# Kernel optimization log

Measured on AMD Instinct MI355X. Metric: run time of the kernel, lower is better.

The kernel has to match this reference:

```python
import jax, jax.numpy as jnp
import numpy as np

HIDDEN = 5120
N_HEADS = 16           # 128 total heads / DEVICE_NUM=8
Q_LORA = 1536
KV_LORA = 512
NOPE = 128
ROPE = 64
QK_DIM = NOPE + ROPE   # 192
V_DIM = 128
EPS = 1e-6
ROPE_BASE = 10000.0
SCALE_BY_DEVICE = 1.0 / 8.0
SOFTMAX_SCALE = QK_DIM ** -0.5
B, S = 1, 2048


def rms_norm(x, w, eps=EPS):
    v = jnp.mean(jnp.square(x), axis=-1, keepdims=True)
    return x * jax.lax.rsqrt(v + eps) * w


def rotate_half(x):
    h = x.shape[-1] // 2
    return jnp.concatenate([-x[..., h:], x[..., :h]], axis=-1)


def interleave(x):
    # DeepSeek rope layout: view(b,h,s,d//2,2).transpose(-1,-2).reshape(b,h,s,d)
    b, h, s, d = x.shape
    return jnp.swapaxes(x.reshape(b, h, s, d // 2, 2), -1, -2).reshape(b, h, s, d)


def setup_inputs() -> dict:
    key = jax.random.key(0)
    ks = jax.random.split(key, 8)
    w = 0.02
    hidden_states = jax.random.normal(ks[0], (B, S, HIDDEN), dtype=jnp.float32)
    position_ids = jnp.arange(S, dtype=jnp.int64 if jax.config.jax_enable_x64 else jnp.int32)[None, :]
    causal = jnp.tril(jnp.ones((S, S), dtype=bool))
    attention_mask = jnp.where(causal, 0.0, -1e9).astype(jnp.float32)[None, None]
    return {
        'hidden_states': hidden_states,
        'position_ids': position_ids,
        'attention_mask': attention_mask,
        'ln_w': jnp.ones((HIDDEN,), jnp.float32),
        'wq_a': jax.random.normal(ks[1], (Q_LORA, HIDDEN), jnp.float32) * w,
        'q_a_ln_w': jnp.ones((Q_LORA,), jnp.float32),
        'wq_b': jax.random.normal(ks[2], (N_HEADS * QK_DIM, Q_LORA), jnp.float32) * w,
        'wkv_a': jax.random.normal(ks[3], (KV_LORA + ROPE, HIDDEN), jnp.float32) * w,
        'kv_a_ln_w': jnp.ones((KV_LORA,), jnp.float32),
        'wkv_b': jax.random.normal(ks[4], (N_HEADS * (NOPE + V_DIM), KV_LORA), jnp.float32) * w,
        'wo': jax.random.normal(ks[5], (HIDDEN, N_HEADS * V_DIM), jnp.float32) * w,
    }


def reference(hidden_states, position_ids, attention_mask, ln_w, wq_a, q_a_ln_w,
              wq_b, wkv_a, kv_a_ln_w, wkv_b, wo):
    b, s, _ = hidden_states.shape
    residual = hidden_states * SCALE_BY_DEVICE
    h = rms_norm(hidden_states, ln_w)

    # Q low-rank decompression: q_a_proj -> RMSNorm -> q_b_proj
    q = rms_norm(h @ wq_a.T, q_a_ln_w) @ wq_b.T
    q = q.reshape(b, s, N_HEADS, QK_DIM).transpose(0, 2, 1, 3)  # b,h,s,192
    q_nope, q_pe = q[..., :NOPE], q[..., NOPE:]

    # KV low-rank: kv_a_proj_with_mqa -> split -> RMSNorm -> kv_b_proj
    ckv = h @ wkv_a.T                                           # b,s,512+64
    c_kv, k_pe = ckv[..., :KV_LORA], ckv[..., KV_LORA:]
    k_pe = k_pe[:, None, :, :]                                  # b,1,s,64
    kv = rms_norm(c_kv, kv_a_ln_w) @ wkv_b.T
    kv = kv.reshape(b, s, N_HEADS, NOPE + V_DIM).transpose(0, 2, 1, 3)
    k_nope, v = kv[..., :NOPE], kv[..., NOPE:]

    # RoPE (DeepSeek interleaved layout)
    inv_freq = 1.0 / (ROPE_BASE ** (jnp.arange(0, ROPE, 2, dtype=jnp.float32) / ROPE))
    freqs = position_ids.astype(jnp.float32)[..., None] * inv_freq  # b,s,32
    emb = jnp.concatenate([freqs, freqs], axis=-1)                  # b,s,64
    cos = jnp.cos(emb)[:, None]                                     # b,1,s,64
    sin = jnp.sin(emb)[:, None]
    q_pe = interleave(q_pe)
    k_pe = interleave(k_pe)
    q_pe = q_pe * cos + rotate_half(q_pe) * sin
    k_pe = k_pe * cos + rotate_half(k_pe) * sin

    k = jnp.concatenate([k_nope, jnp.broadcast_to(k_pe, (b, N_HEADS, s, ROPE))], axis=-1)
    qf = jnp.concatenate([q_nope, q_pe], axis=-1)

    scores = jnp.einsum('bhqd,bhkd->bhqk', qf, k) * SOFTMAX_SCALE + attention_mask
    attn = jax.nn.softmax(scores.astype(jnp.float32), axis=-1).astype(qf.dtype)
    out = jnp.einsum('bhqk,bhkd->bhqd', attn, v)                    # b,h,s,128
    out = out.transpose(0, 2, 1, 3).reshape(b, s, N_HEADS * V_DIM) @ wo.T

    hidden_states = residual + out
    return (hidden_states.astype(jnp.float32), k.astype(jnp.float32), v.astype(jnp.float32))
```

## Files before the change

kernel.cpp:

```cpp
#include <hip/hip_runtime.h>
#include <hip/hip_bf16.h>

typedef __hip_bfloat16 bf16;
typedef __attribute__((ext_vector_type(8))) short bf16x8;
typedef __attribute__((ext_vector_type(4))) float f32x4;

#define S_LEN   2048
#define HIDDEN  5120
#define NHEADS  16
#define QLORA   1536
#define KVLORA  512
#define QKD     192
#define VD      128
#define QN      (NHEADS*QKD)
#define KVN     (NHEADS*(128+VD))
#define QCKN    2112
#define SM_SCALE 0.07216878364870322f

__device__ __forceinline__ f32x4 mfma16(bf16x8 a, bf16x8 b, f32x4 c) {
  return __builtin_amdgcn_mfma_f32_16x16x32_bf16(a, b, c, 0, 0, 0);
}
__device__ __forceinline__ void g2l16(const void* g, void* l) {
  __builtin_amdgcn_global_load_lds((const __attribute__((address_space(1))) void*)g,
                                   (__attribute__((address_space(3))) void*)l, 16, 0, 0);
}
__device__ __forceinline__ bf16x8 ld8(const bf16* p) { return *(const bf16x8*)p; }

__global__ void cvt_multi(const float* s0, bf16* d0, int n0,
                          const float* s1, bf16* d1, int n1,
                          const float* s2, bf16* d2, int n2,
                          const float* s3, bf16* d3, int n3,
                          const float* s4, bf16* d4, int n4s)
{
  int i = blockIdx.x * 256 + threadIdx.x;
  const float* s; bf16* d;
  if (i < n0) { s = s0; d = d0; }
  else if ((i -= n0) < n1) { s = s1; d = d1; }
  else if ((i -= n1) < n2) { s = s2; d = d2; }
  else if ((i -= n2) < n3) { s = s3; d = d3; }
  else if ((i -= n3) < n4s) { s = s4; d = d4; }
  else return;
  const float4 v = ((const float4*)s)[i];
  union { bf16 b[4]; unsigned long long u; } pk;
  pk.b[0] = __float2bfloat16(v.x);
  pk.b[1] = __float2bfloat16(v.y);
  pk.b[2] = __float2bfloat16(v.z);
  pk.b[3] = __float2bfloat16(v.w);
  *(unsigned long long*)(d + (size_t)i * 4) = pk.u;
}

__global__ void rmsnorm_k(const float* __restrict__ in, int istride, int C,
                          const float* __restrict__ w,
                          bf16* __restrict__ out, int ostride)
{
  const int row = blockIdx.x;
  const float* x = in + (size_t)row * istride;
  float ss = 0.f;
  for (int c = threadIdx.x; c < C; c += 256) { float v = x[c]; ss += v * v; }
  #pragma unroll
  for (int m = 32; m >= 1; m >>= 1) ss += __shfl_xor(ss, m, 64);
  __shared__ float red[4];
  if ((threadIdx.x & 63) == 0) red[threadIdx.x >> 6] = ss;
  __syncthreads();
  ss = red[0] + red[1] + red[2] + red[3];
  const float sc = rsqrtf(ss / (float)C + 1e-6f);
  bf16* o = out + (size_t)row * ostride;
  for (int c = threadIdx.x; c < C; c += 256)
    o[c] = __float2bfloat16(x[c] * sc * w[c]);
}

__global__ void rmsnorm2_k(const float* __restrict__ parts,
                           const float* __restrict__ wq, const float* __restrict__ wk,
                           bf16* __restrict__ qa_n, bf16* __restrict__ ckv_n,
                           float* __restrict__ kpe_sum)
{
  const int r = blockIdx.x;
  const bool is_q = r < S_LEN;
  const int row = is_q ? r : r - S_LEN;
  const int C = is_q ? QLORA : KVLORA;
  const size_t PS = (size_t)S_LEN * QCKN;
  const float* x0 = parts + (size_t)row * QCKN + (is_q ? 0 : QLORA);
  const float* w = is_q ? wq : wk;
  bf16* o = (is_q ? qa_n + (size_t)row * QLORA : ckv_n + (size_t)row * KVLORA);
  __shared__ float xs[QLORA];
  float ss = 0.f;
  for (int c = threadIdx.x; c < C; c += 256) {
    const float v = x0[c] + x0[PS + c] + x0[2 * PS + c] + x0[3 * PS + c];
    xs[c] = v;
    ss += v * v;
  }
  #pragma unroll
  for (int m = 32; m >= 1; m >>= 1) ss += __shfl_xor(ss, m, 64);
  __shared__ float red[4];
  if ((threadIdx.x & 63) == 0) red[threadIdx.x >> 6] = ss;
  __syncthreads();
  ss = red[0] + red[1] + red[2] + red[3];
  const float sc = rsqrtf(ss / (float)C + 1e-6f);
  for (int c = threadIdx.x; c < C; c += 256)
    o[c] = __float2bfloat16(xs[c] * sc * w[c]);
  if (!is_q) {
    const float* kp = parts + (size_t)row * QCKN + 2048;
    for (int c = threadIdx.x; c < 64; c += 256)
      kpe_sum[row * 64 + c] = kp[c] + kp[PS + c] + kp[2 * PS + c] + kp[3 * PS + c];
  }
}

template<bool RESID, bool CLAMPN, bool SPLIT>
__global__ __launch_bounds__(256, 4)
void gemm_nt(const bf16* __restrict__ A, const bf16* __restrict__ Bt,
             float* __restrict__ C, int M, int N, int lda, int klen,
             const float* __restrict__ resid, float rscale)
{
  __shared__ bf16 As[2 * 128 * 32];
  __shared__ bf16 Bs[2 * 128 * 32];
  const int tid = threadIdx.x;
  const int wave = tid >> 6;
  const int lane = tid & 63;
  const int l15 = lane & 15, quad = lane >> 4;
  const int bm = blockIdx.x * 128, bn = blockIdx.y * 128;
  const int kbase = blockIdx.z * klen;
  const int wm = (wave >> 1) * 64, wn = (wave & 1) * 64;

  const int srow = tid >> 2;
  const int scol = (((tid & 3) ^ ((tid >> 3) & 3)) << 3);
  const bf16* Ag0 = A + (size_t)(bm + srow) * lda + kbase + scol;
  const bf16* Ag1 = A + (size_t)(bm + 64 + srow) * lda + kbase + scol;
  int bn0 = bn + srow, bn1 = bn + 64 + srow;
  if (CLAMPN) { bn0 = min(bn0, N - 1); bn1 = min(bn1, N - 1); }
  const bf16* Bg0 = Bt + (size_t)bn0 * lda + kbase + scol;
  const bf16* Bg1 = Bt + (size_t)bn1 * lda + kbase + scol;

  char* AsW = (char*)As + wave * 1024;
  char* BsW = (char*)Bs + wave * 1024;

  const int qs = ((quad ^ ((l15 >> 1) & 3)) << 3);

  f32x4 acc[4][4];
  #pragma unroll
  for (int i = 0; i < 4; i++)
    #pragma unroll
    for (int j = 0; j < 4; j++) acc[i][j] = (f32x4){0.f, 0.f, 0.f, 0.f};

  const int nk = klen >> 6;
  for (int kt = 0; kt < nk; ++kt) {
    const int k0 = kt << 6;
    #pragma unroll
    for (int c = 0; c < 2; ++c) {
      g2l16(Ag0 + k0 + c * 32, AsW + c * 8192);
      g2l16(Ag1 + k0 + c * 32, AsW + c * 8192 + 4096);
      g2l16(Bg0 + k0 + c * 32, BsW + c * 8192);
      g2l16(Bg1 + k0 + c * 32, BsW + c * 8192 + 4096);
    }
    __syncthreads();
    #pragma unroll
    for (int c = 0; c < 2; ++c) {
      bf16x8 af[4], bfr[4];
      #pragma unroll
      for (int i = 0; i < 4; i++)
        af[i] = ld8(As + c * 4096 + (wm + i * 16 + l15) * 32 + qs);
      #pragma unroll
      for (int j = 0; j < 4; j++)
        bfr[j] = ld8(Bs + c * 4096 + (wn + j * 16 + l15) * 32 + qs);
      #pragma unroll
      for (int i = 0; i < 4; i++)
        #pragma unroll
        for (int j = 0; j < 4; j++)
          acc[i][j] = mfma16(af[i], bfr[j], acc[i][j]);
    }
    __syncthreads();
  }

  float* Cb = C;
  if (SPLIT) Cb += (size_t)blockIdx.z * ((size_t)S_LEN * (size_t)N);
  #pragma unroll
  for (int i = 0; i < 4; i++)
    #pragma unroll
    for (int j = 0; j < 4; j++) {
      const int row = bm + wm + i * 16 + quad * 4;
      const int col = bn + wn + j * 16 + l15;
      if (!CLAMPN || col < N) {
        #pragma unroll
        for (int r = 0; r < 4; r++) {
          float v = acc[i][j][r];
          const size_t idx = (size_t)(row + r) * N + col;
          if (RESID) v += resid[idx] * rscale;
          Cb[idx] = v;
        }
      }
    }
}

__global__ void rope_assemble_k(
    const float* __restrict__ qp,
    const float* __restrict__ kpe_sum,
    const float* __restrict__ kv,
    const int*   __restrict__ pos,
    float* __restrict__ k_out,
    bf16*  __restrict__ q_bf,
    bf16*  __restrict__ k_bf)
{
  const int s = blockIdx.x;
  const int t = threadIdx.x;
  const size_t QPS = (size_t)S_LEN * QN;
  __shared__ float cs[32], sn[32], kpe[64];
  const float p = (float)pos[s];
  if (t < 32) {
    const float inv = powf(10000.0f, -((float)(2 * t)) / 64.0f);
    const float f = p * inv;
    float si, c;
    sincosf(f, &si, &c);
    cs[t] = c; sn[t] = si;
    const float r0v = kpe_sum[(size_t)s * 64 + 2 * t];
    const float r1v = kpe_sum[(size_t)s * 64 + 2 * t + 1];
    kpe[t]      = r0v * c - r1v * si;
    kpe[32 + t] = r1v * c + r0v * si;
  }
  __syncthreads();
  for (int i = t; i < NHEADS * 128; i += 256) {
    const int h = i >> 7, d = i & 127;
    const size_t o = ((size_t)h * S_LEN + s) * QKD + d;
    const float kn = kv[(size_t)s * KVN + h * 256 + d];
    k_out[o] = kn;
    k_bf[o] = __float2bfloat16(kn);
    const size_t qi = (size_t)s * QN + h * QKD + d;
    q_bf[o] = __float2bfloat16(qp[qi] + qp[QPS + qi]);
  }
  for (int i = t; i < NHEADS * 32; i += 256) {
    const int h = i >> 5, jj = i & 31;
    const size_t qi = (size_t)s * QN + h * QKD + 128 + 2 * jj;
    const float r0v = qp[qi] + qp[QPS + qi];
    const float r1v = qp[qi + 1] + qp[QPS + qi + 1];
    const float c = cs[jj], si = sn[jj];
    const size_t o = ((size_t)h * S_LEN + s) * QKD + 128;
    q_bf[o + jj]      = __float2bfloat16(r0v * c - r1v * si);
    q_bf[o + 32 + jj] = __float2bfloat16(r1v * c + r0v * si);
  }
  for (int i = t; i < NHEADS * 64; i += 256) {
    const int h = i >> 6, jj = i & 63;
    const float v = kpe[jj];
    const size_t o = ((size_t)h * S_LEN + s) * QKD + 128 + jj;
    k_out[o] = v;
    k_bf[o] = __float2bfloat16(v);
  }
}

__global__ void v_transpose_k(const float* __restrict__ kv,
                              float* __restrict__ v_out,
                              bf16* __restrict__ vt_bf)
{
  const int h = blockIdx.x, st = blockIdx.y, dt = blockIdx.z;
  __shared__ float tile[32][33];
  const int tx = threadIdx.x & 31;
  const int ty = (threadIdx.x >> 5) * 4;
  const int s0 = st * 32, d0 = dt * 32;
  #pragma unroll
  for (int r = 0; r < 4; r++) {
    const int sl = ty + r;
    const float v = kv[(size_t)(s0 + sl) * KVN + h * 256 + 128 + d0 + tx];
    v_out[((size_t)h * S_LEN + s0 + sl) * VD + d0 + tx] = v;
    tile[sl][tx] = v;
  }
  __syncthreads();
  #pragma unroll
  for (int r = 0; r < 4; r++) {
    const int dl = ty + r;
    vt_bf[((size_t)h * VD + d0 + dl) * S_LEN + s0 + tx] = __float2bfloat16(tile[tx][dl]);
  }
}

template<bool PARTIAL>
__device__ __forceinline__ void attn_tile(
    const bf16* __restrict__ qh, const bf16* __restrict__ kh,
    const bf16* __restrict__ vh,
    bf16* Ks, bf16* Vs, bf16* Plds,
    int qt, int j0, int j1, int head,
    bf16* __restrict__ aout, float* __restrict__ Op, float* __restrict__ Ml)
{
  const int tid = threadIdx.x;
  const int wave = tid >> 6, lane = tid & 63;
  const int l15 = lane & 15, quad = lane >> 4;
  const int r0 = qt * 64 + wave * 16;

  const int srow = wave * 16 + (lane >> 2);
  const int scol = (lane & 3) * 8;
  const bf16* ksrc = kh + (size_t)srow * QKD + scol;
  bf16* kdst = Ks + srow * 32 + (((lane & 3) ^ ((lane >> 3) & 3)) << 3);
  const int vrow = tid >> 1;
  const int vcol = (tid & 1) * 32;
  const bf16* vsrc = vh + (size_t)vrow * S_LEN + vcol;
  bf16* vdst = Vs + vrow * 72 + vcol;
  const int qs = ((quad ^ ((l15 >> 1) & 3)) << 3);

  bf16x8 qf[6];
  #pragma unroll
  for (int c = 0; c < 6; ++c)
    qf[c] = ld8(qh + (size_t)(r0 + l15) * QKD + c * 32 + quad * 8);

  f32x4 O[8];
  #pragma unroll
  for (int d = 0; d < 8; ++d) O[d] = (f32x4){0.f, 0.f, 0.f, 0.f};
  float mrow[4] = {-1e30f, -1e30f, -1e30f, -1e30f};
  float lrow[4] = {0.f, 0.f, 0.f, 0.f};

  bf16x8 kreg[6], vreg[4];
  #pragma unroll
  for (int c = 0; c < 6; ++c) kreg[c] = ld8(ksrc + (size_t)j0 * 64 * QKD + c * 32);
  #pragma unroll
  for (int c = 0; c < 4; ++c) vreg[c] = ld8(vsrc + (size_t)j0 * 64 + c * 8);

  for (int j = j0; j < j1; ++j) {
    __syncthreads();
    #pragma unroll
    for (int c = 0; c < 6; ++c) *(bf16x8*)(kdst + c * 2048) = kreg[c];
    #pragma unroll
    for (int c = 0; c < 4; ++c) *(bf16x8*)(vdst + c * 8) = vreg[c];
    __syncthreads();
    if (j + 1 < j1) {
      const bf16* src = ksrc + (size_t)(j + 1) * 64 * QKD;
      #pragma unroll
      for (int c = 0; c < 6; ++c) kreg[c] = ld8(src + c * 32);
      const bf16* vs2 = vsrc + (size_t)(j + 1) * 64;
      #pragma unroll
      for (int c = 0; c < 4; ++c) vreg[c] = ld8(vs2 + c * 8);
    }
    const int kc = j * 64;

    f32x4 S[4];
    #pragma unroll
    for (int nt = 0; nt < 4; ++nt) S[nt] = (f32x4){0.f, 0.f, 0.f, 0.f};
    #pragma unroll
    for (int c = 0; c < 6; ++c)
      #pragma unroll
      for (int nt = 0; nt < 4; ++nt) {
        const bf16x8 kf = ld8(Ks + c * 2048 + (nt * 16 + l15) * 32 + qs);
        S[nt] = mfma16(qf[c], kf, S[nt]);
      }

    float mnew[4] = {-1e30f, -1e30f, -1e30f, -1e30f};
    if (j == qt) {
      #pragma unroll
      for (int nt = 0; nt < 4; ++nt) {
        const int col = kc + nt * 16 + l15;
        #pragma unroll
        for (int r = 0; r < 4; r++) {
          const int row = r0 + quad * 4 + r;
          const float v = (col <= row) ? S[nt][r] * SM_SCALE : -1e30f;
          S[nt][r] = v;
          mnew[r] = fmaxf(mnew[r], v);
        }
      }
    } else {
      #pragma unroll
      for (int nt = 0; nt < 4; ++nt)
        #pragma unroll
        for (int r = 0; r < 4; r++) {
          const float v = S[nt][r] * SM_SCALE;
          S[nt][r] = v;
          mnew[r] = fmaxf(mnew[r], v);
        }
    }
    #pragma unroll
    for (int m = 8; m >= 1; m >>= 1)
      #pragma unroll
      for (int r = 0; r < 4; r++)
        mnew[r] = fmaxf(mnew[r], __shfl_xor(mnew[r], m, 64));
    float alpha[4], ladd[4] = {0.f, 0.f, 0.f, 0.f};
    #pragma unroll
    for (int r = 0; r < 4; r++) {
      const float mi = fmaxf(mrow[r], mnew[r]);
      alpha[r] = __expf(mrow[r] - mi);
      mrow[r] = mi;
    }
    #pragma unroll
    for (int nt = 0; nt < 4; ++nt)
      #pragma unroll
      for (int r = 0; r < 4; r++) {
        const float pv = __expf(S[nt][r] - mrow[r]);
        S[nt][r] = pv;
        ladd[r] += pv;
      }
    #pragma unroll
    for (int m = 8; m >= 1; m >>= 1)
      #pragma unroll
      for (int r = 0; r < 4; r++) ladd[r] += __shfl_xor(ladd[r], m, 64);
    #pragma unroll
    for (int r = 0; r < 4; r++) lrow[r] = lrow[r] * alpha[r] + ladd[r];
    #pragma unroll
    for (int d = 0; d < 8; ++d)
      #pragma unroll
      for (int r = 0; r < 4; r++) O[d][r] *= alpha[r];

    #pragma unroll
    for (int nt = 0; nt < 4; ++nt)
      #pragma unroll
      for (int r = 0; r < 4; r++)
        Plds[(wave * 16 + quad * 4 + r) * 72 + nt * 16 + l15] =
            __float2bfloat16(S[nt][r]);

    #pragma unroll
    for (int kt = 0; kt < 2; ++kt) {
      const bf16x8 pf = ld8(Plds + (wave * 16 + l15) * 72 + kt * 32 + quad * 8);
      #pragma unroll
      for (int dt = 0; dt < 8; ++dt) {
        const bf16x8 vf = ld8(Vs + (dt * 16 + l15) * 72 + kt * 32 + quad * 8);
        O[dt] = mfma16(pf, vf, O[dt]);
      }
    }
  }

  if (PARTIAL) {
    #pragma unroll
    for (int dt = 0; dt < 8; ++dt)
      #pragma unroll
      for (int r = 0; r < 4; r++)
        Op[(wave * 16 + quad * 4 + r) * 128 + dt * 16 + l15] = O[dt][r];
    if (l15 == 0) {
      #pragma unroll
      for (int r = 0; r < 4; r++) {
        Ml[wave * 16 + quad * 4 + r] = mrow[r];
        Ml[64 + wave * 16 + quad * 4 + r] = lrow[r];
      }
    }
  } else {
    #pragma unroll
    for (int dt = 0; dt < 8; ++dt) {
      const int col = head * VD + dt * 16 + l15;
      #pragma unroll
      for (int r = 0; r < 4; r++) {
        const int row = r0 + quad * 4 + r;
        aout[(size_t)row * (NHEADS * VD) + col] = __float2bfloat16(O[dt][r] / lrow[r]);
      }
    }
  }
}

__global__ __launch_bounds__(256, 2)
void attn_k(const bf16* __restrict__ qb, const bf16* __restrict__ kb,
            const bf16* __restrict__ vt, bf16* __restrict__ aout,
            float* __restrict__ Opart, float* __restrict__ Mlpart)
{
  __shared__ bf16 Ks[6 * 64 * 32];
  __shared__ bf16 Vs[128 * 72];
  __shared__ bf16 Plds[4 * 16 * 72];

  const int lin = blockIdx.x;
  const int xcd = lin & 7;
  const int t = lin >> 3;
  const int head = xcd * 2 + (t >> 5);
  const int rem = t & 31;
  const int b = rem >> 1;
  const int role = rem & 1;
  const int qtl = b, qth = 31 - b;
  const int pi = head * 16 + (15 - b);

  const bf16* qh = qb + (size_t)head * S_LEN * QKD;
  const bf16* kh = kb + (size_t)head * S_LEN * QKD;
  const bf16* vh = vt + (size_t)head * VD * S_LEN;

  if (role == 0) {
    attn_tile<true>(qh, kh, vh, Ks, Vs, Plds, qth, 0, 16, head, aout,
                    Opart + (size_t)pi * 8192, Mlpart + (size_t)pi * 128);
  } else {
    attn_tile<false>(qh, kh, vh, Ks, Vs, Plds, qtl, 0, qtl + 1, head, aout,
                     nullptr, nullptr);
    attn_tile<true>(qh, kh, vh, Ks, Vs, Plds, qth, 16, qth + 1, head, aout,
                    Opart + (size_t)(256 + pi) * 8192,
                    Mlpart + (size_t)(256 + pi) * 128);
  }
}

__global__ void merge_k(const float* __restrict__ Opart,
                        const float* __restrict__ Mlpart,
                        bf16* __restrict__ aout)
{
  const int pi = blockIdx.x;
  const int head = pi >> 4;
  const int qth = (pi & 15) + 16;
  const int tid = threadIdx.x;
  const int r = tid >> 2;
  const int d0 = (tid & 3) * 32;
  const float mA = Mlpart[(size_t)pi * 128 + r];
  const float lA = Mlpart[(size_t)pi * 128 + 64 + r];
  const float mB = Mlpart[(size_t)(256 + pi) * 128 + r];
  const float lB = Mlpart[(size_t)(256 + pi) * 128 + 64 + r];
  const float m = fmaxf(mA, mB);
  const float fa = __expf(mA - m), fb = __expf(mB - m);
  const float inv = 1.f / (lA * fa + lB * fb);
  const float4* OA = (const float4*)(Opart + (size_t)pi * 8192 + r * 128 + d0);
  const float4* OB = (const float4*)(Opart + (size_t)(256 + pi) * 8192 + r * 128 + d0);
  bf16* out = aout + (size_t)(qth * 64 + r) * (NHEADS * VD) + head * VD + d0;
  #pragma unroll
  for (int i = 0; i < 8; ++i) {
    const float4 va = OA[i], vb = OB[i];
    union { bf16 h[4]; unsigned long long u; } pk;
    pk.h[0] = __float2bfloat16((va.x * fa + vb.x * fb) * inv);
    pk.h[1] = __float2bfloat16((va.y * fa + vb.y * fb) * inv);
    pk.h[2] = __float2bfloat16((va.z * fa + vb.z * fb) * inv);
    pk.h[3] = __float2bfloat16((va.w * fa + vb.w * fb) * inv);
    *(unsigned long long*)(out + i * 4) = pk.u;
  }
}

extern "C" void kernel_launch(void* const* d_in, const int* in_sizes, int n_in,
                              void* d_out, int out_size, void* d_ws, size_t ws_size,
                              hipStream_t stream)
{
  const float* hs      = (const float*)d_in[0];
  const int*   pos     = (const int*)  d_in[1];
  const float* ln_w    = (const float*)d_in[3];
  const float* wq_a    = (const float*)d_in[4];
  const float* q_a_ln  = (const float*)d_in[5];
  const float* wq_b    = (const float*)d_in[6];
  const float* wkv_a   = (const float*)d_in[7];
  const float* kv_a_ln = (const float*)d_in[8];
  const float* wkv_b   = (const float*)d_in[9];
  const float* wo      = (const float*)d_in[10];

  float* out_hidden = (float*)d_out;
  float* out_k = out_hidden + (size_t)S_LEN * HIDDEN;
  float* out_v = out_k + (size_t)NHEADS * S_LEN * QKD;

  char* ws = (char*)d_ws;
  size_t off = 0;
  auto alloc = [&](size_t bytes) { char* p = ws + off; off += (bytes + 255) & ~255ULL; return p; };

  bf16* h_b     = (bf16*)alloc((size_t)S_LEN * HIDDEN * 2);
  bf16* w1_b    = (bf16*)alloc((size_t)QCKN * HIDDEN * 2);
  bf16* wqb_b   = (bf16*)alloc((size_t)QN * QLORA * 2);
  bf16* wkvb_b  = (bf16*)alloc((size_t)KVN * KVLORA * 2);
  bf16* wo_b    = (bf16*)alloc((size_t)HIDDEN * (NHEADS * VD) * 2);
  char* region  = alloc((size_t)2 * S_LEN * QN * 4 + (size_t)S_LEN * KVN * 4);
  float* qa_parts = (float*)region;
  float* q_f      = (float*)region;
  float* kv_f     = (float*)(region + (size_t)2 * S_LEN * QN * 4);
  float* Opart    = (float*)region;
  float* Mlpart   = (float*)(region + (size_t)512 * 8192 * 4);
  float* kpe_sum = (float*)alloc((size_t)S_LEN * 64 * 4);
  bf16* qa_n    = (bf16*)alloc((size_t)S_LEN * QLORA * 2);
  bf16* ckv_n   = (bf16*)alloc((size_t)S_LEN * KVLORA * 2);
  bf16* q_bf    = (bf16*)alloc((size_t)NHEADS * S_LEN * QKD * 2);
  bf16* k_bf    = (bf16*)alloc((size_t)NHEADS * S_LEN * QKD * 2);
  bf16* vt_bf   = (bf16*)alloc((size_t)NHEADS * VD * S_LEN * 2);
  bf16* attn_b  = (bf16*)alloc((size_t)S_LEN * (NHEADS * VD) * 2);

  {
    const int n0 = (QLORA * HIDDEN) / 4;
    const int n1 = ((QCKN - QLORA) * HIDDEN) / 4;
    const int n2 = (QN * QLORA) / 4;
    const int n3 = (KVN * KVLORA) / 4;
    const int n4s = (HIDDEN * NHEADS * VD) / 4;
    const int tot = n0 + n1 + n2 + n3 + n4s;
    cvt_multi<<<(tot + 255) / 256, 256, 0, stream>>>(
        wq_a, w1_b, n0,
        wkv_a, w1_b + (size_t)QLORA * HIDDEN, n1,
        wq_b, wqb_b, n2,
        wkv_b, wkvb_b, n3,
        wo, wo_b, n4s);
  }

  rmsnorm_k<<<S_LEN, 256, 0, stream>>>(hs, HIDDEN, HIDDEN, ln_w, h_b, HIDDEN);

  gemm_nt<false, true, true><<<dim3(16, 17, 4), 256, 0, stream>>>(
      h_b, w1_b, qa_parts, S_LEN, QCKN, HIDDEN, HIDDEN / 4, nullptr, 0.f);

  rmsnorm2_k<<<2 * S_LEN, 256, 0, stream>>>(qa_parts, q_a_ln, kv_a_ln,
                                            qa_n, ckv_n, kpe_sum);

  gemm_nt<false, false, true><<<dim3(16, QN / 128, 2), 256, 0, stream>>>(
      qa_n, wqb_b, q_f, S_LEN, QN, QLORA, QLORA / 2, nullptr, 0.f);
  gemm_nt<false, false, false><<<dim3(16, KVN / 128, 1), 256, 0, stream>>>(
      ckv_n, wkvb_b, kv_f, S_LEN, KVN, KVLORA, KVLORA, nullptr, 0.f);

  rope_assemble_k<<<S_LEN, 256, 0, stream>>>(q_f, kpe_sum, kv_f, pos,
                                             out_k, q_bf, k_bf);
  v_transpose_k<<<dim3(NHEADS, S_LEN / 32, VD / 32), 256, 0, stream>>>(kv_f, out_v, vt_bf);

  attn_k<<<dim3(512), 256, 0, stream>>>(q_bf, k_bf, vt_bf, attn_b, Opart, Mlpart);
  merge_k<<<dim3(256), 256, 0, stream>>>(Opart, Mlpart, attn_b);

  gemm_nt<true, false, false><<<dim3(16, HIDDEN / 128, 1), 256, 0, stream>>>(
      attn_b, wo_b, out_hidden, S_LEN, HIDDEN, NHEADS * VD, NHEADS * VD, hs, 0.125f);

  (void)in_sizes; (void)n_in; (void)out_size; (void)ws_size;
}
```

Before: 519.3 us.

## Double-buffer GEMM LDS tiles to overlap global loads with MFMA compute

Measured after the change: 545.5 us. +5.0%, slower.

```diff
diff --git a/kernel.cpp b/kernel.cpp
--- a/kernel.cpp
+++ b/kernel.cpp
@@ -25,6 +25,13 @@
                                    (__attribute__((address_space(3))) void*)l, 16, 0, 0);
 }
 __device__ __forceinline__ bf16x8 ld8(const bf16* p) { return *(const bf16x8*)p; }
+
+__device__ __forceinline__ void bar() {
+  __builtin_amdgcn_sched_barrier(0);
+  __builtin_amdgcn_s_barrier();
+  __builtin_amdgcn_sched_barrier(0);
+}
+#define VMCNT(n) asm volatile("s_waitcnt vmcnt(" #n ")" ::: "memory")
 
 __global__ void cvt_multi(const float* s0, bf16* d0, int n0,
                           const float* s1, bf16* d1, int n1,
@@ -106,13 +113,13 @@
 }
 
 template<bool RESID, bool CLAMPN, bool SPLIT>
-__global__ __launch_bounds__(256, 4)
+__global__ __launch_bounds__(256, 2)
 void gemm_nt(const bf16* __restrict__ A, const bf16* __restrict__ Bt,
              float* __restrict__ C, int M, int N, int lda, int klen,
              const float* __restrict__ resid, float rscale)
 {
-  __shared__ bf16 As[2 * 128 * 32];
-  __shared__ bf16 Bs[2 * 128 * 32];
+  __shared__ bf16 As[2 * 2 * 128 * 32];
+  __shared__ bf16 Bs[2 * 2 * 128 * 32];
   const int tid = threadIdx.x;
   const int wave = tid >> 6;
   const int lane = tid & 63;
@@ -141,33 +148,48 @@
     #pragma unroll
     for (int j = 0; j < 4; j++) acc[i][j] = (f32x4){0.f, 0.f, 0.f, 0.f};
 
+  auto stage = [&](int kt, int buf) {
+    const int k0 = kt << 6;
+    char* Ad = AsW + buf * 16384;
+    char* Bd = BsW + buf * 16384;
+    #pragma unroll
+    for (int c = 0; c < 2; ++c) {
+      g2l16(Ag0 + k0 + c * 32, Ad + c * 8192);
+      g2l16(Ag1 + k0 + c * 32, Ad + c * 8192 + 4096);
+      g2l16(Bg0 + k0 + c * 32, Bd + c * 8192);
+      g2l16(Bg1 + k0 + c * 32, Bd + c * 8192 + 4096);
+    }
+  };
+
   const int nk = klen >> 6;
+  stage(0, 0);
   for (int kt = 0; kt < nk; ++kt) {
-    const int k0 = kt << 6;
-    #pragma unroll
-    for (int c = 0; c < 2; ++c) {
-      g2l16(Ag0 + k0 + c * 32, AsW + c * 8192);
-      g2l16(Ag1 + k0 + c * 32, AsW + c * 8192 + 4096);
-      g2l16(Bg0 + k0 + c * 32, BsW + c * 8192);
-      g2l16(Bg1 + k0 + c * 32, BsW + c * 8192 + 4096);
-    }
-    __syncthreads();
+    const int buf = kt & 1;
+    if (kt + 1 < nk) {
+      stage(kt + 1, buf ^ 1);
+      VMCNT(8);
+    } else {
+      VMCNT(0);
+    }
+    bar();
+    const bf16* Asb = As + buf * 8192;
+    const bf16* Bsb = Bs + buf * 8192;
     #pragma unroll
     for (int c = 0; c < 2; ++c) {
       bf16x8 af[4], bfr[4];
       #pragma unroll
       for (int i = 0; i < 4; i++)
-        af[i] = ld8(As + c * 4096 + (wm + i * 16 + l15) * 32 + qs);
+        af[i] = ld8(Asb + c * 4096 + (wm + i * 16 + l15) * 32 + qs);
       #pragma unroll
       for (int j = 0; j < 4; j++)
-        bfr[j] = ld8(Bs + c * 4096 + (wn + j * 16 + l15) * 32 + qs);
+        bfr[j] = ld8(Bsb + c * 4096 + (wn + j * 16 + l15) * 32 + qs);
       #pragma unroll
       for (int i = 0; i < 4; i++)
         #pragma unroll
         for (int j = 0; j < 4; j++)
           acc[i][j] = mfma16(af[i], bfr[j], acc[i][j]);
     }
-    __syncthreads();
+    bar();
   }
 
   float* Cb = C;
```

## Flatten GEMM grids with XCD-aware block mapping, merge Q/KV GEMMs, load V directly

Applied to the files above, without the earlier changes.

Measured after the change: 576.3 us. 11.0% more time.

```diff
diff --git a/kernel.cpp b/kernel.cpp
--- a/kernel.cpp
+++ b/kernel.cpp
@@ -105,30 +105,47 @@
   }
 }
 
-template<bool RESID, bool CLAMPN, bool SPLIT>
+struct GP {
+  const bf16* A; const bf16* Bt; float* C;
+  const float* resid; float rscale;
+  int lda;
+  int nby;
+  int klen;
+  int N;
+  int flags;
+};
+
 __global__ __launch_bounds__(256, 4)
-void gemm_nt(const bf16* __restrict__ A, const bf16* __restrict__ Bt,
-             float* __restrict__ C, int M, int N, int lda, int klen,
-             const float* __restrict__ resid, float rscale)
+void gemm_flat(GP p0, GP p1, int nb0, int q8)
 {
   __shared__ bf16 As[2 * 128 * 32];
   __shared__ bf16 Bs[2 * 128 * 32];
+  const int orig = blockIdx.x;
+  int wg = (orig & 7) * q8 + (orig >> 3);
+  GP p = p0;
+  if (wg >= nb0) { p = p1; wg -= nb0; }
+  const int bm = (wg & 15) << 7;
+  const unsigned rest = (unsigned)wg >> 4;
+  const unsigned nby = (unsigned)p.nby;
+  const int bn = (int)(rest % nby) << 7;
+  const int z = (int)(rest / nby);
+  const int lda = p.lda, N = p.N;
+  const int kbase = z * p.klen;
+
   const int tid = threadIdx.x;
   const int wave = tid >> 6;
   const int lane = tid & 63;
   const int l15 = lane & 15, quad = lane >> 4;
-  const int bm = blockIdx.x * 128, bn = blockIdx.y * 128;
-  const int kbase = blockIdx.z * klen;
   const int wm = (wave >> 1) * 64, wn = (wave & 1) * 64;
 
   const int srow = tid >> 2;
   const int scol = (((tid & 3) ^ ((tid >> 3) & 3)) << 3);
-  const bf16* Ag0 = A + (size_t)(bm + srow) * lda + kbase + scol;
-  const bf16* Ag1 = A + (size_t)(bm + 64 + srow) * lda + kbase + scol;
-  int bn0 = bn + srow, bn1 = bn + 64 + srow;
-  if (CLAMPN) { bn0 = min(bn0, N - 1); bn1 = min(bn1, N - 1); }
-  const bf16* Bg0 = Bt + (size_t)bn0 * lda + kbase + scol;
-  const bf16* Bg1 = Bt + (size_t)bn1 * lda + kbase + scol;
+  const bf16* Ag0 = p.A + (size_t)(bm + srow) * lda + kbase + scol;
+  const bf16* Ag1 = Ag0 + (size_t)64 * lda;
+  const int bn0 = min(bn + srow, N - 1);
+  const int bn1 = min(bn + 64 + srow, N - 1);
+  const bf16* Bg0 = p.Bt + (size_t)bn0 * lda + kbase + scol;
+  const bf16* Bg1 = p.Bt + (size_t)bn1 * lda + kbase + scol;
 
   char* AsW = (char*)As + wave * 1024;
   char* BsW = (char*)Bs + wave * 1024;
@@ -141,7 +158,7 @@
     #pragma unroll
     for (int j = 0; j < 4; j++) acc[i][j] = (f32x4){0.f, 0.f, 0.f, 0.f};
 
-  const int nk = klen >> 6;
+  const int nk = p.klen >> 6;
   for (int kt = 0; kt < nk; ++kt) {
     const int k0 = kt << 6;
     #pragma unroll
@@ -170,20 +187,20 @@
     __syncthreads();
   }
 
-  float* Cb = C;
-  if (SPLIT) Cb += (size_t)blockIdx.z * ((size_t)S_LEN * (size_t)N);
+  float* Cb = p.C + (size_t)z * ((size_t)S_LEN * (size_t)N);
+  const bool rs = p.flags != 0;
   #pragma unroll
   for (int i = 0; i < 4; i++)
     #pragma unroll
     for (int j = 0; j < 4; j++) {
       const int row = bm + wm + i * 16 + quad * 4;
       const int col = bn + wn + j * 16 + l15;
-      if (!CLAMPN || col < N) {
+      if (col < N) {
         #pragma unroll
         for (int r = 0; r < 4; r++) {
           float v = acc[i][j][r];
           const size_t idx = (size_t)(row + r) * N + col;
-          if (RESID) v += resid[idx] * rscale;
+          if (rs) v += p.resid[idx] * p.rscale;
           Cb[idx] = v;
         }
       }
@@ -272,7 +289,7 @@
 __device__ __forceinline__ void attn_tile(
     const bf16* __restrict__ qh, const bf16* __restrict__ kh,
     const bf16* __restrict__ vh,
-    bf16* Ks, bf16* Vs, bf16* Plds,
+    bf16* Ks, bf16* Plds,
     int qt, int j0, int j1, int head,
     bf16* __restrict__ aout, float* __restrict__ Op, float* __restrict__ Ml)
 {
@@ -285,11 +302,8 @@
   const int scol = (lane & 3) * 8;
   const bf16* ksrc = kh + (size_t)srow * QKD + scol;
   bf16* kdst = Ks + srow * 32 + (((lane & 3) ^ ((lane >> 3) & 3)) << 3);
-  const int vrow = tid >> 1;
-  const int vcol = (tid & 1) * 32;
-  const bf16* vsrc = vh + (size_t)vrow * S_LEN + vcol;
-  bf16* vdst = Vs + vrow * 72 + vcol;
   const int qs = ((quad ^ ((l15 >> 1) & 3)) << 3);
+  const bf16* vfb = vh + (size_t)l15 * S_LEN + quad * 8;
 
   bf16x8 qf[6];
   #pragma unroll
@@ -302,28 +316,29 @@
   float mrow[4] = {-1e30f, -1e30f, -1e30f, -1e30f};
   float lrow[4] = {0.f, 0.f, 0.f, 0.f};
 
-  bf16x8 kreg[6], vreg[4];
+  bf16x8 kreg[6];
   #pragma unroll
   for (int c = 0; c < 6; ++c) kreg[c] = ld8(ksrc + (size_t)j0 * 64 * QKD + c * 32);
-  #pragma unroll
-  for (int c = 0; c < 4; ++c) vreg[c] = ld8(vsrc + (size_t)j0 * 64 + c * 8);
 
   for (int j = j0; j < j1; ++j) {
     __syncthreads();
     #pragma unroll
     for (int c = 0; c < 6; ++c) *(bf16x8*)(kdst + c * 2048) = kreg[c];
-    #pragma unroll
-    for (int c = 0; c < 4; ++c) *(bf16x8*)(vdst + c * 8) = vreg[c];
     __syncthreads();
+    const int kc = j * 64;
+
+    bf16x8 vf[2][8];
+    #pragma unroll
+    for (int kt = 0; kt < 2; ++kt)
+      #pragma unroll
+      for (int dt = 0; dt < 8; ++dt)
+        vf[kt][dt] = ld8(vfb + (size_t)dt * 16 * S_LEN + kc + kt * 32);
+
     if (j + 1 < j1) {
       const bf16* src = ksrc + (size_t)(j + 1) * 64 * QKD;
       #pragma unroll
       for (int c = 0; c < 6; ++c) kreg[c] = ld8(src + c * 32);
-      const bf16* vs2 = vsrc + (size_t)(j + 1) * 64;
-      #pragma unroll
-      for (int c = 0; c < 4; ++c) vreg[c] = ld8(vs2 + c * 8);
-    }
-    const int kc = j * 64;
+    }
 
     f32x4 S[4];
     #pragma unroll
@@ -401,10 +416,8 @@
     for (int kt = 0; kt < 2; ++kt) {
       const bf16x8 pf = ld8(Plds + (wave * 16 + l15) * 72 + kt * 32 + quad * 8);
       #pragma unroll
-      for (int dt = 0; dt < 8; ++dt) {
-        const bf16x8 vf = ld8(Vs + (dt * 16 + l15) * 72 + kt * 32 + quad * 8);
-        O[dt] = mfma16(pf, vf, O[dt]);
-      }
+      for (int dt = 0; dt < 8; ++dt)
+        O[dt] = mfma16(pf, vf[kt][dt], O[dt]);
     }
   }
 
@@ -440,7 +453,6 @@
             float* __restrict__ Opart, float* __restrict__ Mlpart)
 {
   __shared__ bf16 Ks[6 * 64 * 32];
-  __shared__ bf16 Vs[128 * 72];
   __shared__ bf16 Plds[4 * 16 * 72];
 
   const int lin = blockIdx.x;
@@ -458,12 +470,12 @@
   const bf16* vh = vt + (size_t)head * VD * S_LEN;
 
   if (role == 0) {
-    attn_tile<true>(qh, kh, vh, Ks, Vs, Plds, qth, 0, 16, head, aout,
+    attn_tile<true>(qh, kh, vh, Ks, Plds, qth, 0, 16, head, aout,
                     Opart + (size_t)pi * 8192, Mlpart + (size_t)pi * 128);
   } else {
-    attn_tile<false>(qh, kh, vh, Ks, Vs, Plds, qtl, 0, qtl + 1, head, aout,
+    attn_tile<false>(qh, kh, vh, Ks, Plds, qtl, 0, qtl + 1, head, aout,
                      nullptr, nullptr);
-    attn_tile<true>(qh, kh, vh, Ks, Vs, Plds, qth, 16, qth + 1, head, aout,
+    attn_tile<true>(qh, kh, vh, Ks, Plds, qth, 16, qth + 1, head, aout,
                     Opart + (size_t)(256 + pi) * 8192,
                     Mlpart + (size_t)(256 + pi) * 128);
   }
@@ -560,16 +572,19 @@
 
   rmsnorm_k<<<S_LEN, 256, 0, stream>>>(hs, HIDDEN, HIDDEN, ln_w, h_b, HIDDEN);
 
-  gemm_nt<false, true, true><<<dim3(16, 17, 4), 256, 0, stream>>>(
-      h_b, w1_b, qa_parts, S_LEN, QCKN, HIDDEN, HIDDEN / 4, nullptr, 0.f);
+  {
+    GP g1 = {h_b, w1_b, qa_parts, nullptr, 0.f, HIDDEN, 17, HIDDEN / 4, QCKN, 0};
+    gemm_flat<<<dim3(1088), 256, 0, stream>>>(g1, g1, 1088, 136);
+  }
 
   rmsnorm2_k<<<2 * S_LEN, 256, 0, stream>>>(qa_parts, q_a_ln, kv_a_ln,
                                             qa_n, ckv_n, kpe_sum);
 
-  gemm_nt<false, false, true><<<dim3(16, QN / 128, 2), 256, 0, stream>>>(
-      qa_n, wqb_b, q_f, S_LEN, QN, QLORA, QLORA / 2, nullptr, 0.f);
-  gemm_nt<false, false, false><<<dim3(16, KVN / 128, 1), 256, 0, stream>>>(
-      ckv_n, wkvb_b, kv_f, S_LEN, KVN, KVLORA, KVLORA, nullptr, 0.f);
+  {
+    GP g2 = {qa_n, wqb_b, q_f, nullptr, 0.f, QLORA, 24, QLORA / 2, QN, 0};
+    GP g3 = {ckv_n, wkvb_b, kv_f, nullptr, 0.f, KVLORA, 32, KVLORA, KVN, 0};
+    gemm_flat<<<dim3(1280), 256, 0, stream>>>(g2, g3, 768, 160);
+  }
 
   rope_assemble_k<<<S_LEN, 256, 0, stream>>>(q_f, kpe_sum, kv_f, pos,
                                              out_k, q_bf, k_bf);
@@ -578,8 +593,10 @@
   attn_k<<<dim3(512), 256, 0, stream>>>(q_bf, k_bf, vt_bf, attn_b, Opart, Mlpart);
   merge_k<<<dim3(256), 256, 0, stream>>>(Opart, Mlpart, attn_b);
 
-  gemm_nt<true, false, false><<<dim3(16, HIDDEN / 128, 1), 256, 0, stream>>>(
-      attn_b, wo_b, out_hidden, S_LEN, HIDDEN, NHEADS * VD, NHEADS * VD, hs, 0.125f);
+  {
+    GP g4 = {attn_b, wo_b, out_hidden, hs, 0.125f, NHEADS * VD, 40, NHEADS * VD, HIDDEN, 1};
+    gemm_flat<<<dim3(640), 256, 0, stream>>>(g4, g4, 640, 80);
+  }
 
   (void)in_sizes; (void)n_in; (void)out_size; (void)ws_size;
 }
```
